# Kernel tuning notes

Measured on AMD Instinct MI355X. Metric: run time of the kernel, lower is better.

## Reference

```python
import jax, jax.numpy as jnp
import numpy as np

EMBED_DIM = 1024
NUM_HEADS = 16
HEAD_DIM = EMBED_DIM // NUM_HEADS
VOCAB = 5          # languages
BOTTLENECK = 800
SCALING = HEAD_DIM ** -0.5


def setup_inputs() -> dict:
    key = jax.random.key(0)
    ks = jax.random.split(key, 16)
    T, B, D = 2048, 2, EMBED_DIM
    s = 0.02
    return {
        "query": jax.random.normal(ks[0], (T, B, D), jnp.float32),
        "key": jax.random.normal(ks[1], (T, B, D), jnp.float32),
        "value": jax.random.normal(ks[2], (T, B, D), jnp.float32),
        "wq": jax.random.normal(ks[3], (D, D), jnp.float32) * s,
        "bq": jnp.zeros((D,), jnp.float32),
        "wk": jax.random.normal(ks[4], (D, D), jnp.float32) * s,
        "bk": jnp.zeros((D,), jnp.float32),
        "wv": jax.random.normal(ks[5], (D, D), jnp.float32) * s,
        "bv": jnp.zeros((D,), jnp.float32),
        "wo": jax.random.normal(ks[6], (D, D), jnp.float32) * s,
        "bo": jnp.zeros((D,), jnp.float32),
        "wte": jax.random.normal(ks[7], (VOCAB, D), jnp.float32) * s,
        "ct_w1": jax.random.normal(ks[8], (VOCAB, BOTTLENECK, D), jnp.float32) * s,
        "ct_b1": jnp.zeros((VOCAB, BOTTLENECK), jnp.float32),
        "ct_w2": jax.random.normal(ks[9], (VOCAB, 2 * D, BOTTLENECK), jnp.float32) * s,
        "ct_b2": jnp.zeros((VOCAB, 2 * D), jnp.float32),
        "language_id": jax.random.randint(ks[10], (B,), 0, VOCAB, jnp.int32),
    }


def _prefix_kv(language_id, wte, ct_w1, ct_b1, ct_w2, ct_b2):
    # PrefixTuningLangEmbLangspec: embed lang id, run all 5 bottleneck MLPs,
    # select per-sample MLP output via one-hot weighting, split into K/V.
    B = language_id.shape[0]
    emb = wte[language_id]                                  # [B, D]
    h = jnp.tanh(jnp.einsum("bd,chd->cbh", emb, ct_w1) + ct_b1[:, None, :])  # [5,B,800]
    kv = jnp.einsum("cbh,cdh->cbd", h, ct_w2) + ct_b2[:, None, :]            # [5,B,2D]
    w = jax.nn.one_hot(language_id, VOCAB, dtype=kv.dtype)  # [B,5]
    kv_sel = jnp.einsum("bc,cbd->bd", w, kv)                # [B,2D]
    # view(b,1,2,nh,hd): first D -> keys, second D -> values
    pk = kv_sel[:, :EMBED_DIM].reshape(B, NUM_HEADS, 1, HEAD_DIM)
    pv = kv_sel[:, EMBED_DIM:].reshape(B, NUM_HEADS, 1, HEAD_DIM)
    return pk, pv


def reference(query, key, value, wq, bq, wk, bk, wv, bv, wo, bo,
              wte, ct_w1, ct_b1, ct_w2, ct_b2, language_id):
    T, B, D = query.shape
    pk, pv = _prefix_kv(language_id, wte, ct_w1, ct_b1, ct_w2, ct_b2)  # [B,H,1,hd]

    # separate Q/K/V projections (Linear: x @ W^T + b)
    q = (jnp.einsum("tbd,ed->tbe", query, wq) + bq) * SCALING
    k = jnp.einsum("tbd,ed->tbe", key, wk) + bk
    v = jnp.einsum("tbd,ed->tbe", value, wv) + bv

    # [T,B,D] -> [B,H,T,hd]
    def split_heads(x):
        return x.reshape(T, B, NUM_HEADS, HEAD_DIM).transpose(1, 2, 0, 3)

    qh = split_heads(q)
    kh = jnp.concatenate([pk, split_heads(k)], axis=2)  # [B,H,T+1,hd]
    vh = jnp.concatenate([pv, split_heads(v)], axis=2)

    scores = jnp.einsum("bhqd,bhkd->bhqk", qh, kh)      # [B,H,T,T+1]
    attn = jax.nn.softmax(scores, axis=-1)
    ctx = jnp.einsum("bhqk,bhkd->bhqd", attn, vh)       # [B,H,T,hd]

    ctx = ctx.transpose(2, 0, 1, 3).reshape(T, B, D)    # back to [T,B,D]
    out = jnp.einsum("tbd,ed->tbe", ctx, wo) + bo
    return out
```

## Files before the change

kernel.cpp:

```cpp
#include <hip/hip_runtime.h>
#include <stdint.h>

#define T_SEQ 2048
#define BATCH 2
#define DIM   1024
#define NH    16
#define HD    64
#define TKP   2112

typedef _Float16 v8h __attribute__((ext_vector_type(8)));
typedef _Float16 v4h __attribute__((ext_vector_type(4)));
typedef float    f32x4 __attribute__((ext_vector_type(4)));
typedef float    f32x16 __attribute__((ext_vector_type(16)));

__device__ __forceinline__ void gload16(const _Float16* g, _Float16* l) {
  __builtin_amdgcn_global_load_lds(
      (__attribute__((address_space(1))) unsigned int*)g,
      (__attribute__((address_space(3))) unsigned int*)l, 16, 0, 0);
}

__global__ void cvt_all(const float4* __restrict__ s0, const float4* __restrict__ s1,
                        const float4* __restrict__ s2, const float4* __restrict__ s3,
                        const float4* __restrict__ s4, const float4* __restrict__ s5,
                        const float4* __restrict__ s6,
                        v4h* __restrict__ d0, v4h* __restrict__ d1, v4h* __restrict__ d2,
                        v4h* __restrict__ d3, v4h* __restrict__ d4, v4h* __restrict__ d5,
                        v4h* __restrict__ d6) {
  const int NTB4 = 1048576, DD4 = 262144;
  int i = blockIdx.x * 256 + threadIdx.x;
  const float4* s; v4h* d; int off;
  if (i < 3 * NTB4) {
    int t = i / NTB4; off = i - t * NTB4;
    s = t == 0 ? s0 : t == 1 ? s1 : s2;
    d = t == 0 ? d0 : t == 1 ? d1 : d2;
  } else {
    int j = i - 3 * NTB4;
    int t = j / DD4; off = j - t * DD4;
    s = t == 0 ? s3 : t == 1 ? s4 : t == 2 ? s5 : s6;
    d = t == 0 ? d3 : t == 1 ? d4 : t == 2 ? d5 : d6;
  }
  float4 v = s[off];
  v4h o = { (_Float16)v.x, (_Float16)v.y, (_Float16)v.z, (_Float16)v.w };
  d[off] = o;
}

__global__ void prefix_pad_k(const float* __restrict__ wte, const float* __restrict__ w1,
                             const float* __restrict__ b1, const int* __restrict__ lang,
                             float* __restrict__ hbuf,
                             _Float16* __restrict__ kb, _Float16* __restrict__ vb) {
  if (blockIdx.x >= 400) {
    int bh = blockIdx.x - 400;
    v8h z = {};
    _Float16* kp = kb + ((size_t)bh * TKP + 2048) * 64;
    for (int i = threadIdx.x; i < 512; i += 256) *(v8h*)&kp[i * 8] = z;
    for (int i = threadIdx.x; i < 512; i += 256) {
      int c = i >> 3, seg = i & 7;
      *(v8h*)&vb[((size_t)bh * 64 + c) * TKP + 2048 + seg * 8] = z;
    }
    return;
  }
  int wid = blockIdx.x * 4 + (threadIdx.x >> 6);
  int lane = threadIdx.x & 63;
  int b = wid / 800, j = wid - b * 800;
  int c = lang[b];
  const float* wr = w1 + ((size_t)c * 800 + j) * 1024;
  const float* em = wte + (size_t)c * 1024;
  float s = 0.f;
  for (int d = lane; d < 1024; d += 64) s += wr[d] * em[d];
  for (int off = 32; off > 0; off >>= 1) s += __shfl_down(s, off, 64);
  if (lane == 0) hbuf[wid] = tanhf(s + b1[c * 800 + j]);
}

__global__ void prefix_kv_k(const float* __restrict__ w2, const float* __restrict__ b2,
                            const float* __restrict__ hbuf, const int* __restrict__ lang,
                            _Float16* __restrict__ kb, _Float16* __restrict__ vb) {
  int wid = blockIdx.x * 4 + (threadIdx.x >> 6);
  int lane = threadIdx.x & 63;
  int b = wid >> 11, e = wid & 2047;
  int c = lang[b];
  const float* wr = w2 + ((size_t)c * 2048 + e) * 800;
  const float* hb = hbuf + b * 800;
  float s = 0.f;
  for (int j = lane; j < 800; j += 64) s += wr[j] * hb[j];
  for (int off = 32; off > 0; off >>= 1) s += __shfl_down(s, off, 64);
  if (lane == 0) {
    float val = s + b2[c * 2048 + e];
    if (e < 1024) {
      int h = e >> 6, hd = e & 63;
      kb[((size_t)(b * 16 + h) * TKP + 2048) * 64 + hd] = (_Float16)val;
    } else {
      int d = e - 1024;
      int h = d >> 6, hd = d & 63;
      vb[((size_t)(b * 16 + h) * 64 + hd) * TKP + 2048] = (_Float16)val;
    }
  }
}

__global__ __launch_bounds__(256) void gemm_bt_k(
    const _Float16* __restrict__ A0, const _Float16* __restrict__ A1, const _Float16* __restrict__ A2,
    const _Float16* __restrict__ W0, const _Float16* __restrict__ W1, const _Float16* __restrict__ W2,
    const float* __restrict__ bs0, const float* __restrict__ bs1, const float* __restrict__ bs2,
    _Float16* __restrict__ qb, _Float16* __restrict__ kb, _Float16* __restrict__ vb,
    float* __restrict__ fout, int mode_base)
{
  __shared__ __align__(16) _Float16 smem[128 * 64 * 2];
  _Float16* As = smem;
  _Float16* Bs = smem + 128 * 64;
  const int mode = mode_base + blockIdx.z;
  const _Float16* A = (mode == 1) ? A1 : (mode == 2) ? A2 : A0;
  const _Float16* W = (mode == 1) ? W1 : (mode == 2) ? W2 : W0;
  const float* bias = (mode == 1) ? bs1 : (mode == 2) ? bs2 : bs0;
  const int tid = threadIdx.x, w = tid >> 6, lane = tid & 63;
  const int quad = lane >> 4, l15 = lane & 15;
  const int r0 = blockIdx.x * 128, c0 = blockIdx.y * 128;
  const int wm = w >> 1, wn = w & 1;
  const int srow = lane >> 3, sseg = lane & 7;
  f32x4 acc[4][4] = {};
  for (int k0 = 0; k0 < 1024; k0 += 64) {
    for (int i = 0; i < 4; ++i) {
      int rowb = w * 32 + i * 8;
      gload16(A + (size_t)(r0 + rowb + srow) * 1024 + k0 + sseg * 8, &As[rowb * 64]);
      gload16(W + (size_t)(c0 + rowb + srow) * 1024 + k0 + sseg * 8, &Bs[rowb * 64]);
    }
    __syncthreads();
    for (int ks = 0; ks < 2; ++ks) {
      v8h af[4], bfr[4];
      for (int mt = 0; mt < 4; ++mt)
        af[mt] = *(const v8h*)&As[(wm * 64 + mt * 16 + l15) * 64 + ks * 32 + quad * 8];
      for (int nt = 0; nt < 4; ++nt)
        bfr[nt] = *(const v8h*)&Bs[(wn * 64 + nt * 16 + l15) * 64 + ks * 32 + quad * 8];
      for (int mt = 0; mt < 4; ++mt)
        for (int nt = 0; nt < 4; ++nt)
          acc[mt][nt] = __builtin_amdgcn_mfma_f32_16x16x32_f16(af[mt], bfr[nt], acc[mt][nt], 0, 0, 0);
    }
    __syncthreads();
  }
  if (mode == 3) {
    for (int nt = 0; nt < 4; ++nt) {
      int e = c0 + wn * 64 + nt * 16 + l15;
      float be = bias[e];
      for (int mt = 0; mt < 4; ++mt) {
        int rb = r0 + wm * 64 + mt * 16 + quad * 4;
        for (int reg = 0; reg < 4; ++reg)
          fout[(size_t)(rb + reg) * 1024 + e] = acc[mt][nt][reg] + be;
      }
    }
    return;
  }
  _Float16* st = smem + w * 4096;
  const float qscale = (mode == 0) ? 0.125f * 1.44269504088896341f : 1.0f;
  for (int p = 0; p < 2; ++p) {
    __syncthreads();
    for (int ntl = 0; ntl < 2; ++ntl) {
      int nt = p * 2 + ntl;
      int e = c0 + wn * 64 + nt * 16 + l15;
      float be = bias[e];
      for (int mt = 0; mt < 4; ++mt)
        for (int reg = 0; reg < 4; ++reg) {
          float val = (acc[mt][nt][reg] + be) * qscale;
          int rl = mt * 16 + quad * 4 + reg;
          if (mode != 2) st[rl * 40 + ntl * 16 + l15] = (_Float16)val;
          else st[(ntl * 16 + l15) * 72 + (rl & 1) * 32 + (rl >> 1)] = (_Float16)val;
        }
    }
    __syncthreads();
    if (mode != 2) {
      for (int it = 0; it < 4; ++it) {
        int chunk = it * 64 + lane;
        int rr = chunk >> 2, seg = chunk & 3;
        v8h val = *(const v8h*)&st[rr * 40 + seg * 8];
        int r = r0 + wm * 64 + rr, b = r & 1, t = r >> 1;
        int e0 = c0 + wn * 64 + p * 32 + seg * 8;
        int h = e0 >> 6, hd0 = e0 & 63;
        if (mode == 0) *(v8h*)&qb[((size_t)(b * 16 + h) * 2048 + t) * 64 + hd0] = val;
        else           *(v8h*)&kb[((size_t)(b * 16 + h) * TKP + t) * 64 + hd0] = val;
      }
    } else {
      for (int it = 0; it < 4; ++it) {
        int chunk = it * 64 + lane;
        int el = chunk >> 3, b = (chunk >> 2) & 1, qs = chunk & 3;
        v8h val = *(const v8h*)&st[el * 72 + b * 32 + qs * 8];
        int e = c0 + wn * 64 + p * 32 + el;
        int h = e >> 6, hd = e & 63;
        int t0 = ((r0 + wm * 64) >> 1) + qs * 8;
        *(v8h*)&vb[((size_t)(b * 16 + h) * 64 + hd) * TKP + t0] = val;
      }
    }
  }
}

__global__ __launch_bounds__(256) void attn_k(
    const _Float16* __restrict__ qb, const _Float16* __restrict__ kb,
    const _Float16* __restrict__ vb, _Float16* __restrict__ ctx)
{
  __shared__ __align__(16) _Float16 Ks[2][64 * 72];
  __shared__ __align__(16) _Float16 Vs[2][64 * 72];
  const int bh = blockIdx.x;
  const int qt0 = blockIdx.y * 128;
  const int tid = threadIdx.x, w = tid >> 6, lane = tid & 63;
  const int l31 = lane & 31, h8 = (lane >> 5) * 8;
  v8h qf[4];
#pragma unroll
  for (int t = 0; t < 4; ++t)
    qf[t] = *(const v8h*)(qb + ((size_t)bh * 2048 + qt0 + w * 32 + l31) * 64 + t * 16 + h8);
  const int sr = tid >> 3, sseg = tid & 7;
  const _Float16* kptr = kb + (size_t)bh * TKP * 64 + sr * 64 + sseg * 8;
  const _Float16* vptr = vb + (size_t)bh * 64 * TKP + (size_t)sr * TKP + sseg * 8;
  int4 kp0 = *(const int4*)kptr, kp1 = *(const int4*)(kptr + 2048);
  int4 vp0 = *(const int4*)vptr, vp1 = *(const int4*)(vptr + 32 * TKP);
  kptr += 4096; vptr += 64;
  const int vcb = (sseg >> 1) * 32 + (sseg & 1) * 8;
  f32x16 O0 = {}, O1 = {};
  float l_ = 0.f;
  for (int kc = 0; kc < 33; ++kc) {
    _Float16* Kb = Ks[kc & 1];
    _Float16* Vb = Vs[kc & 1];
    *(int4*)&Kb[sr * 72 + sseg * 8] = kp0;
    *(int4*)&Kb[(sr + 32) * 72 + sseg * 8] = kp1;
    {
      char* vr0 = (char*)&Vb[sr * 72];
      char* vr1 = (char*)&Vb[(sr + 32) * 72];
      *(int2*)(vr0 + vcb)      = *(int2*)&vp0;
      *(int2*)(vr0 + vcb + 16) = *((int2*)&vp0 + 1);
      *(int2*)(vr1 + vcb)      = *(int2*)&vp1;
      *(int2*)(vr1 + vcb + 16) = *((int2*)&vp1 + 1);
    }
    __syncthreads();
    if (kc < 32) {
      kp0 = *(const int4*)kptr; kp1 = *(const int4*)(kptr + 2048);
      vp0 = *(const int4*)vptr; vp1 = *(const int4*)(vptr + 32 * TKP);
      kptr += 4096; vptr += 64;
    }
    f32x16 S0 = {}, S1 = {};
    __builtin_amdgcn_s_setprio(1);
#pragma unroll
    for (int t = 0; t < 4; ++t) {
      v8h kf0 = *(const v8h*)&Kb[(l31) * 72 + t * 16 + h8];
      v8h kf1 = *(const v8h*)&Kb[(32 + l31) * 72 + t * 16 + h8];
      S0 = __builtin_amdgcn_mfma_f32_32x32x16_f16(kf0, qf[t], S0, 0, 0, 0);
      S1 = __builtin_amdgcn_mfma_f32_32x32x16_f16(kf1, qf[t], S1, 0, 0, 0);
    }
    __builtin_amdgcn_s_setprio(0);
    if (kc == 32) {
#pragma unroll
      for (int r = 0; r < 16; ++r) {
        if (r > 0) S0[r] = -1e30f;
        S1[r] = -1e30f;
      }
      if (lane >= 32) S0[0] = -1e30f;
    }
    float rs = 0.f;
#pragma unroll
    for (int r = 0; r < 16; ++r) { S0[r] = __builtin_amdgcn_exp2f(S0[r]); rs += S0[r]; }
#pragma unroll
    for (int r = 0; r < 16; ++r) { S1[r] = __builtin_amdgcn_exp2f(S1[r]); rs += S1[r]; }
    l_ += rs;
    __builtin_amdgcn_s_setprio(1);
#pragma unroll
    for (int c = 0; c < 4; ++c) {
      v8h ph;
      if (c == 0)      ph = (v8h){ (_Float16)S0[0], (_Float16)S0[1], (_Float16)S0[2], (_Float16)S0[3],
                                   (_Float16)S0[4], (_Float16)S0[5], (_Float16)S0[6], (_Float16)S0[7] };
      else if (c == 1) ph = (v8h){ (_Float16)S0[8], (_Float16)S0[9], (_Float16)S0[10], (_Float16)S0[11],
                                   (_Float16)S0[12], (_Float16)S0[13], (_Float16)S0[14], (_Float16)S0[15] };
      else if (c == 2) ph = (v8h){ (_Float16)S1[0], (_Float16)S1[1], (_Float16)S1[2], (_Float16)S1[3],
                                   (_Float16)S1[4], (_Float16)S1[5], (_Float16)S1[6], (_Float16)S1[7] };
      else             ph = (v8h){ (_Float16)S1[8], (_Float16)S1[9], (_Float16)S1[10], (_Float16)S1[11],
                                   (_Float16)S1[12], (_Float16)S1[13], (_Float16)S1[14], (_Float16)S1[15] };
      v8h vf0 = *(const v8h*)&Vb[(l31) * 72 + c * 16 + h8];
      v8h vf1 = *(const v8h*)&Vb[(32 + l31) * 72 + c * 16 + h8];
      O0 = __builtin_amdgcn_mfma_f32_32x32x16_f16(vf0, ph, O0, 0, 0, 0);
      O1 = __builtin_amdgcn_mfma_f32_32x32x16_f16(vf1, ph, O1, 0, 0, 0);
    }
    __builtin_amdgcn_s_setprio(0);
  }
  l_ += __shfl_xor(l_, 32, 64);
  const float inv = 1.f / l_;
  const int b = bh >> 4, hh = bh & 15;
  const int q = qt0 + w * 32 + l31;
  _Float16* cbase = ctx + ((size_t)q * 2 + b) * 1024 + hh * 64 + (h8 >> 1);
#pragma unroll
  for (int rq = 0; rq < 4; ++rq) {
    v4h o0 = { (_Float16)(O0[rq * 4 + 0] * inv), (_Float16)(O0[rq * 4 + 1] * inv),
               (_Float16)(O0[rq * 4 + 2] * inv), (_Float16)(O0[rq * 4 + 3] * inv) };
    *(v4h*)(cbase + rq * 8) = o0;
    v4h o1 = { (_Float16)(O1[rq * 4 + 0] * inv), (_Float16)(O1[rq * 4 + 1] * inv),
               (_Float16)(O1[rq * 4 + 2] * inv), (_Float16)(O1[rq * 4 + 3] * inv) };
    *(v4h*)(cbase + 32 + rq * 8) = o1;
  }
}

extern "C" void kernel_launch(void* const* d_in, const int* in_sizes, int n_in,
                              void* d_out, int out_size, void* d_ws, size_t ws_size,
                              hipStream_t stream) {
  (void)in_sizes; (void)n_in; (void)out_size; (void)ws_size;
  const float* query = (const float*)d_in[0];
  const float* key_  = (const float*)d_in[1];
  const float* value = (const float*)d_in[2];
  const float* wq = (const float*)d_in[3];
  const float* bq = (const float*)d_in[4];
  const float* wk = (const float*)d_in[5];
  const float* bk = (const float*)d_in[6];
  const float* wv = (const float*)d_in[7];
  const float* bv = (const float*)d_in[8];
  const float* wo = (const float*)d_in[9];
  const float* bo = (const float*)d_in[10];
  const float* wte = (const float*)d_in[11];
  const float* w1 = (const float*)d_in[12];
  const float* b1 = (const float*)d_in[13];
  const float* w2 = (const float*)d_in[14];
  const float* b2 = (const float*)d_in[15];
  const int* lang = (const int*)d_in[16];
  float* out = (float*)d_out;

  const size_t NTB = (size_t)T_SEQ * BATCH * DIM;
  const size_t DD  = (size_t)DIM * DIM;
  const size_t KVN = (size_t)BATCH * NH * TKP * HD;
  _Float16* xq  = (_Float16*)d_ws;
  _Float16* xk  = xq + NTB;
  _Float16* xv  = xk + NTB;
  _Float16* wqb = xv + NTB;
  _Float16* wkb = wqb + DD;
  _Float16* wvb = wkb + DD;
  _Float16* wob = wvb + DD;
  _Float16* qbuf = wob + DD;
  _Float16* kbuf = qbuf + NTB;
  _Float16* vbuf = kbuf + KVN;
  float* hbuf = (float*)(vbuf + KVN);
  _Float16* ctxb = xq;

  cvt_all<<<16384, 256, 0, stream>>>((const float4*)query, (const float4*)key_,
                                     (const float4*)value, (const float4*)wq,
                                     (const float4*)wk, (const float4*)wv, (const float4*)wo,
                                     (v4h*)xq, (v4h*)xk, (v4h*)xv, (v4h*)wqb,
                                     (v4h*)wkb, (v4h*)wvb, (v4h*)wob);
  prefix_pad_k<<<432, 256, 0, stream>>>(wte, w1, b1, lang, hbuf, kbuf, vbuf);
  prefix_kv_k<<<1024, 256, 0, stream>>>(w2, b2, hbuf, lang, kbuf, vbuf);
  gemm_bt_k<<<dim3(32, 8, 3), 256, 0, stream>>>(xq, xk, xv, wqb, wkb, wvb, bq, bk, bv,
                                                qbuf, kbuf, vbuf, nullptr, 0);
  attn_k<<<dim3(32, 16), 256, 0, stream>>>(qbuf, kbuf, vbuf, ctxb);
  gemm_bt_k<<<dim3(32, 8, 1), 256, 0, stream>>>(ctxb, ctxb, ctxb, wob, wob, wob, bo, bo, bo,
                                                qbuf, kbuf, vbuf, out, 3);
}
```

Measured before the change: 298.0 us.

## Double-buffer GEMM LDS tiles with async prefetch and XOR swizzle

The projection GEMM now stages the next K-tile into a second LDS buffer with global_load_lds while MFMAs run on the current one, gated by explicit vmcnt waits and raw s_barrier. The LDS layout is also XOR-swizzled per row so that fragment reads avoid bank conflicts. This aims to hide global-load latency and LDS conflicts in the QKV and output projections. The cost is doubled LDS use, which can lower occupancy, and the hand-written waitcnt and barrier ordering carries correctness risk.

New measurement: 276.4 us. 1.08x faster.

```diff
diff --git a/kernel.cpp b/kernel.cpp
--- a/kernel.cpp
+++ b/kernel.cpp
@@ -103,9 +103,7 @@
     _Float16* __restrict__ qb, _Float16* __restrict__ kb, _Float16* __restrict__ vb,
     float* __restrict__ fout, int mode_base)
 {
-  __shared__ __align__(16) _Float16 smem[128 * 64 * 2];
-  _Float16* As = smem;
-  _Float16* Bs = smem + 128 * 64;
+  __shared__ __align__(16) _Float16 smem[2][128 * 64 * 2];
   const int mode = mode_base + blockIdx.z;
   const _Float16* A = (mode == 1) ? A1 : (mode == 2) ? A2 : A0;
   const _Float16* W = (mode == 1) ? W1 : (mode == 2) ? W2 : W0;
@@ -115,25 +113,50 @@
   const int r0 = blockIdx.x * 128, c0 = blockIdx.y * 128;
   const int wm = w >> 1, wn = w & 1;
   const int srow = lane >> 3, sseg = lane & 7;
+  const int sw_seg = sseg ^ srow;
+  const int rsw = l15 & 7;
   f32x4 acc[4][4] = {};
-  for (int k0 = 0; k0 < 1024; k0 += 64) {
+
+  auto stage = [&](int k0, int p) {
+    _Float16* As = smem[p];
+    _Float16* Bs = smem[p] + 8192;
+#pragma unroll
     for (int i = 0; i < 4; ++i) {
       int rowb = w * 32 + i * 8;
-      gload16(A + (size_t)(r0 + rowb + srow) * 1024 + k0 + sseg * 8, &As[rowb * 64]);
-      gload16(W + (size_t)(c0 + rowb + srow) * 1024 + k0 + sseg * 8, &Bs[rowb * 64]);
-    }
-    __syncthreads();
+      gload16(A + (size_t)(r0 + rowb + srow) * 1024 + k0 + sw_seg * 8, &As[rowb * 64]);
+      gload16(W + (size_t)(c0 + rowb + srow) * 1024 + k0 + sw_seg * 8, &Bs[rowb * 64]);
+    }
+  };
+
+  stage(0, 0);
+  for (int t = 0; t < 16; ++t) {
+    if (t < 15) {
+      stage((t + 1) << 6, (t + 1) & 1);
+      asm volatile("s_waitcnt vmcnt(8)" ::: "memory");
+    } else {
+      asm volatile("s_waitcnt vmcnt(0)" ::: "memory");
+    }
+    __builtin_amdgcn_s_barrier();
+    __builtin_amdgcn_sched_barrier(0);
+    const _Float16* As = smem[t & 1];
+    const _Float16* Bs = smem[t & 1] + 8192;
+#pragma unroll
     for (int ks = 0; ks < 2; ++ks) {
       v8h af[4], bfr[4];
+#pragma unroll
       for (int mt = 0; mt < 4; ++mt)
-        af[mt] = *(const v8h*)&As[(wm * 64 + mt * 16 + l15) * 64 + ks * 32 + quad * 8];
+        af[mt] = *(const v8h*)&As[(wm * 64 + mt * 16 + l15) * 64 + (((ks * 4 + quad) ^ rsw) * 8)];
+#pragma unroll
       for (int nt = 0; nt < 4; ++nt)
-        bfr[nt] = *(const v8h*)&Bs[(wn * 64 + nt * 16 + l15) * 64 + ks * 32 + quad * 8];
+        bfr[nt] = *(const v8h*)&Bs[(wn * 64 + nt * 16 + l15) * 64 + (((ks * 4 + quad) ^ rsw) * 8)];
+#pragma unroll
       for (int mt = 0; mt < 4; ++mt)
+#pragma unroll
         for (int nt = 0; nt < 4; ++nt)
           acc[mt][nt] = __builtin_amdgcn_mfma_f32_16x16x32_f16(af[mt], bfr[nt], acc[mt][nt], 0, 0, 0);
     }
-    __syncthreads();
+    __builtin_amdgcn_sched_barrier(0);
+    __builtin_amdgcn_s_barrier();
   }
   if (mode == 3) {
     for (int nt = 0; nt < 4; ++nt) {
@@ -147,7 +170,7 @@
     }
     return;
   }
-  _Float16* st = smem + w * 4096;
+  _Float16* st = &smem[0][0] + w * 4096;
   const float qscale = (mode == 0) ? 0.125f * 1.44269504088896341f : 1.0f;
   for (int p = 0; p < 2; ++p) {
     __syncthreads();
```
